# Kernel tuning notes

Hardware: AMD Instinct MI355X
Metric: run time of the kernel (lower is better)

The kernel has to match this reference:

```python
import jax, jax.numpy as jnp
import numpy as np

E = 8        # n_experts
K = 2        # top-k
DIM = 1024
HID = 2048   # swiglu hidden; fc1 out = 2*HID
B, T = 4, 2048


def setup_inputs() -> dict:
    key = jax.random.key(0)
    ks = jax.random.split(key, 7)
    s = 0.02
    return {
        "x": jax.random.normal(ks[0], (B, T, DIM), dtype=jnp.float32),
        "router_w": jax.random.normal(ks[1], (E, DIM), dtype=jnp.float32) * s,
        "router_b": jnp.zeros((E,), dtype=jnp.float32),
        "W1": jax.random.normal(ks[2], (E, DIM, 2 * HID), dtype=jnp.float32) * s,
        "b1": jnp.zeros((E, 2 * HID), dtype=jnp.float32),
        "W2": jax.random.normal(ks[3], (E, HID, DIM), dtype=jnp.float32) * s,
        "b2": jnp.zeros((E, DIM), dtype=jnp.float32),
    }


def _swiglu(h):
    h1, h2 = jnp.split(h, 2, axis=-1)
    return jax.nn.silu(h1) * h2


def reference(x, router_w, router_b, W1, b1, W2, b2):
    # Router: logits = Linear(dim, E), temperature = 1.0
    logits = jnp.einsum("btd,ed->bte", x, router_w) + router_b  # [B,T,E]
    topk_val, topk_idx = jax.lax.top_k(logits, K)               # [B,T,K]
    weights = jax.nn.softmax(topk_val, axis=-1)                 # softmax router
    # combine[b,t,e] = sum_k weights[b,t,k] * [topk_idx[b,t,k] == e]
    combine = jnp.sum(jax.nn.one_hot(topk_idx, E, dtype=x.dtype)
                      * weights[..., None], axis=-2)            # [B,T,E]
    out = jnp.zeros_like(x)
    # Fixed small loop over experts (structurally distinct weight slices).
    for e in range(E):
        h = jnp.einsum("btd,dh->bth", x, W1[e]) + b1[e]         # [B,T,2H]
        y = jnp.einsum("bth,hd->btd", _swiglu(h), W2[e]) + b2[e]
        out = out + combine[..., e:e + 1] * y
    return out
```

## Files before the change

### kernel.cpp

```cpp
#include <hip/hip_runtime.h>
#include <stdint.h>

typedef unsigned short u16;

#define E_    8
#define DIM_  1024
#define HID_  2048
#define H2_   4096
#define NTOK  8192
#define RTOK  32

typedef __attribute__((ext_vector_type(8))) short bf16x8;
typedef __attribute__((ext_vector_type(4))) float f32x4;

__device__ __forceinline__ u16 f2bf(float f) {
  uint32_t u = __builtin_bit_cast(uint32_t, f);
  uint32_t r = (u + 0x7FFFu + ((u >> 16) & 1u)) >> 16;
  return (u16)r;
}
__device__ __forceinline__ float bf2f(u16 u) {
  return __builtin_bit_cast(float, (uint32_t)u << 16);
}

__device__ __forceinline__ void gload16(const void* g, void* l) {
  __builtin_amdgcn_global_load_lds(
      (const __attribute__((address_space(1))) void*)g,
      (__attribute__((address_space(3))) void*)l, 16, 0, 0);
}


__global__ void cvt_x(const float* __restrict__ x, u16* __restrict__ xb, int n8) {
  int i = blockIdx.x * blockDim.x + threadIdx.x;
  if (i >= n8) return;
  const float4* p = (const float4*)(x + (size_t)i * 8);
  float4 a = p[0], b = p[1];
  union { u16 u[8]; uint4 v; } r;
  r.u[0] = f2bf(a.x); r.u[1] = f2bf(a.y); r.u[2] = f2bf(a.z); r.u[3] = f2bf(a.w);
  r.u[4] = f2bf(b.x); r.u[5] = f2bf(b.y); r.u[6] = f2bf(b.z); r.u[7] = f2bf(b.w);
  *(uint4*)(xb + (size_t)i * 8) = r.v;
}

__global__ void tconv(const float* __restrict__ src, u16* __restrict__ dst, int R, int C) {
  __shared__ float t[64][65];
  int e = blockIdx.z;
  int r0 = blockIdx.y * 64, c0 = blockIdx.x * 64;
  const float* s = src + (size_t)e * R * C;
  u16* d = dst + (size_t)e * R * C;
  int tid = threadIdx.x;
  int rr = tid >> 4, cc = (tid & 15) * 4;
#pragma unroll
  for (int p = 0; p < 4; ++p) {
    float4 v = *(const float4*)(s + (size_t)(r0 + p * 16 + rr) * C + c0 + cc);
    t[p * 16 + rr][cc + 0] = v.x; t[p * 16 + rr][cc + 1] = v.y;
    t[p * 16 + rr][cc + 2] = v.z; t[p * 16 + rr][cc + 3] = v.w;
  }
  __syncthreads();
  int cr = tid >> 3, rc = (tid & 7) * 8;
#pragma unroll
  for (int p = 0; p < 2; ++p) {
    union { u16 u[8]; uint4 v; } w;
#pragma unroll
    for (int j = 0; j < 8; ++j) w.u[j] = f2bf(t[rc + j][p * 32 + cr]);
    *(uint4*)(d + (size_t)(c0 + p * 32 + cr) * R + r0 + rc) = w.v;
  }
}


__global__ void router(const float* __restrict__ x, const float* __restrict__ rw,
                       const float* __restrict__ rb, int* __restrict__ counts,
                       int* __restrict__ btok, float* __restrict__ bw,
                       int* __restrict__ tokrec) {
  __shared__ float srw[E_ * DIM_];
  __shared__ float sb[E_];
  __shared__ int   hcnt[E_], hbase[E_];
  __shared__ int   te[RTOK * 2];
  __shared__ float twt[RTOK * 2];
  __shared__ int   tloc[RTOK * 2];

  int tid = threadIdx.x;
  for (int i = tid; i < E_ * DIM_ / 4; i += 256)
    ((float4*)srw)[i] = ((const float4*)rw)[i];
  if (tid < E_) { sb[tid] = rb[tid]; hcnt[tid] = 0; }
  __syncthreads();

  int wid = tid >> 6, lane = tid & 63;
#pragma unroll
  for (int s = 0; s < RTOK / 4; ++s) {
    int lt = wid * (RTOK / 4) + s;
    int t = blockIdx.x * RTOK + lt;
    const float* xt = x + (size_t)t * DIM_;
    float acc[8] = {0.f, 0.f, 0.f, 0.f, 0.f, 0.f, 0.f, 0.f};
#pragma unroll
    for (int it = 0; it < 4; ++it) {
      int d = it * 256 + lane * 4;
      float4 xv = *(const float4*)(xt + d);
#pragma unroll
      for (int e = 0; e < 8; ++e) {
        float4 rv = *(const float4*)(&srw[e * DIM_ + d]);
        acc[e] += xv.x * rv.x + xv.y * rv.y + xv.z * rv.z + xv.w * rv.w;
      }
    }
#pragma unroll
    for (int e = 0; e < 8; ++e)
#pragma unroll
      for (int off = 32; off; off >>= 1)
        acc[e] += __shfl_xor(acc[e], off, 64);
    if (lane == 0) {
      float v[8];
#pragma unroll
      for (int e = 0; e < 8; ++e) v[e] = acc[e] + sb[e];
      int i0 = 0;
#pragma unroll
      for (int e = 1; e < 8; ++e) if (v[e] > v[i0]) i0 = e;
      int i1 = (i0 == 0) ? 1 : 0;
#pragma unroll
      for (int e = 0; e < 8; ++e) if (e != i0 && v[e] > v[i1]) i1 = e;
      float w0 = 1.f / (1.f + expf(v[i1] - v[i0]));
      float w1 = 1.f - w0;
      int l0 = atomicAdd(&hcnt[i0], 1);
      int l1 = atomicAdd(&hcnt[i1], 1);
      te[lt * 2 + 0] = i0; twt[lt * 2 + 0] = w0; tloc[lt * 2 + 0] = l0;
      te[lt * 2 + 1] = i1; twt[lt * 2 + 1] = w1; tloc[lt * 2 + 1] = l1;
    }
  }
  __syncthreads();
  if (tid < E_) hbase[tid] = atomicAdd(&counts[tid], hcnt[tid]);
  __syncthreads();
  if (tid < RTOK * 2) {
    int e = te[tid];
    int p = hbase[e] + tloc[tid];
    int t = blockIdx.x * RTOK + (tid >> 1);
    btok[e * NTOK + p] = t;
    bw[e * NTOK + p] = twt[tid];
    tokrec[t * 2 + (tid & 1)] = (e << 13) | p;
  }
}


__launch_bounds__(256, 4)
__global__ void gemm1(const u16* __restrict__ xb, const u16* __restrict__ w1t,
                      const float* __restrict__ b1, const int* __restrict__ counts,
                      const int* __restrict__ btok, u16* __restrict__ hb) {
  int e = blockIdx.z, mblk = blockIdx.y, nblk = blockIdx.x;
  int cnt = counts[e];
  if (mblk * 128 >= cnt) return;
  int base = 0;
#pragma unroll
  for (int i = 0; i < 8; ++i) base += (i < e) ? counts[i] : 0;

  __shared__ u16 lA[128 * 64];
  __shared__ u16 lB[128 * 64];
  __shared__ int sTok[128];

  int tid = threadIdx.x, wid = tid >> 6, lane = tid & 63;
  if (tid < 128) {
    int gr = mblk * 128 + tid;
    sTok[tid] = (gr < cnt) ? btok[e * NTOK + gr] : btok[e * NTOK];
  }
  __syncthreads();

  f32x4 acc[4][4] = {};
  int wr = wid >> 1, wc = wid & 1;
  int l15 = lane & 15, lhi = lane >> 4;
  const size_t w1e = (size_t)e * H2_ * DIM_;

  int segsw = ((lane & 7) ^ ((lane >> 3) & 7)) * 8;
  const u16* gA[4];
  const u16* gB[4];
#pragma unroll
  for (int i = 0; i < 4; ++i) {
    int r = wid * 32 + i * 8 + (lane >> 3);
    gA[i] = xb + (size_t)sTok[r] * DIM_ + segsw;
    int gcol = nblk * 64 + (r >> 6) * 32 + (r & 31) + ((r >> 5) & 1) * 2048;
    gB[i] = w1t + w1e + (size_t)gcol * DIM_ + segsw;
  }
  int rxor = (l15 & 7) * 8;

  for (int kt = 0; kt < DIM_ / 64; ++kt) {
#pragma unroll
    for (int i = 0; i < 4; ++i)
      gload16(gA[i] + kt * 64, &lA[(wid * 32 + i * 8) * 64]);
#pragma unroll
    for (int i = 0; i < 4; ++i)
      gload16(gB[i] + kt * 64, &lB[(wid * 32 + i * 8) * 64]);
    __syncthreads();
#pragma unroll
    for (int ks = 0; ks < 2; ++ks) {
      int segrd = ((ks * 4 + lhi) * 8) ^ rxor;
      bf16x8 a[4], b[4];
#pragma unroll
      for (int m = 0; m < 4; ++m)
        a[m] = *(const bf16x8*)&lA[(wr * 64 + m * 16 + l15) * 64 + segrd];
#pragma unroll
      for (int n = 0; n < 4; ++n)
        b[n] = *(const bf16x8*)&lB[(wc * 64 + n * 16 + l15) * 64 + segrd];
#pragma unroll
      for (int m = 0; m < 4; ++m)
#pragma unroll
        for (int n = 0; n < 4; ++n)
          acc[m][n] = __builtin_amdgcn_mfma_f32_16x16x32_bf16(a[m], b[n], acc[m][n], 0, 0, 0);
    }
    __syncthreads();
  }

#pragma unroll
  for (int n = 0; n < 2; ++n) {
    int outcol = nblk * 64 + wc * 32 + n * 16 + l15;
    float bb1 = b1[e * H2_ + outcol];
    float bb2 = b1[e * H2_ + outcol + HID_];
#pragma unroll
    for (int m = 0; m < 4; ++m) {
#pragma unroll
      for (int j = 0; j < 4; ++j) {
        int rt = wr * 64 + m * 16 + lhi * 4 + j;
        int gr = mblk * 128 + rt;
        if (gr < cnt) {
          float h1 = acc[m][n][j] + bb1;
          float h2 = acc[m][n + 2][j] + bb2;
          float s = (h1 / (1.f + __expf(-h1))) * h2;
          hb[(size_t)(base + gr) * HID_ + outcol] = f2bf(s);
        }
      }
    }
  }
}


__launch_bounds__(256, 4)
__global__ void gemm2(const u16* __restrict__ hb, const u16* __restrict__ w2t,
                      const float* __restrict__ b2, const int* __restrict__ counts,
                      const float* __restrict__ bw, u16* __restrict__ ybuf) {
  int e = blockIdx.z, mblk = blockIdx.y, nblk = blockIdx.x;
  int cnt = counts[e];
  if (mblk * 128 >= cnt) return;
  int base = 0;
#pragma unroll
  for (int i = 0; i < 8; ++i) base += (i < e) ? counts[i] : 0;

  __shared__ u16 lA[128 * 64];
  __shared__ u16 lB[128 * 64];
  __shared__ float sW[128];

  int tid = threadIdx.x, wid = tid >> 6, lane = tid & 63;
  if (tid < 128) {
    int gr = mblk * 128 + tid;
    sW[tid] = (gr < cnt) ? bw[e * NTOK + gr] : 0.f;
  }
  __syncthreads();

  f32x4 acc[4][4] = {};
  int wr = wid >> 1, wc = wid & 1;
  int l15 = lane & 15, lhi = lane >> 4;

  int segsw = ((lane & 7) ^ ((lane >> 3) & 7)) * 8;
  const u16* gA[4];
  const u16* gB[4];
#pragma unroll
  for (int i = 0; i < 4; ++i) {
    int r = wid * 32 + i * 8 + (lane >> 3);
    gA[i] = hb + (size_t)(base + mblk * 128 + r) * HID_ + segsw;
    gB[i] = w2t + (size_t)e * DIM_ * HID_ + (size_t)(nblk * 128 + r) * HID_ + segsw;
  }
  int rxor = (l15 & 7) * 8;

  for (int kt = 0; kt < HID_ / 64; ++kt) {
#pragma unroll
    for (int i = 0; i < 4; ++i) {
      gload16(gA[i] + kt * 64, &lA[(wid * 32 + i * 8) * 64]);
      gload16(gB[i] + kt * 64, &lB[(wid * 32 + i * 8) * 64]);
    }
    __syncthreads();
#pragma unroll
    for (int ks = 0; ks < 2; ++ks) {
      int segrd = ((ks * 4 + lhi) * 8) ^ rxor;
      bf16x8 a[4], b[4];
#pragma unroll
      for (int m = 0; m < 4; ++m)
        a[m] = *(const bf16x8*)&lA[(wr * 64 + m * 16 + l15) * 64 + segrd];
#pragma unroll
      for (int n = 0; n < 4; ++n)
        b[n] = *(const bf16x8*)&lB[(wc * 64 + n * 16 + l15) * 64 + segrd];
#pragma unroll
      for (int m = 0; m < 4; ++m)
#pragma unroll
        for (int n = 0; n < 4; ++n)
          acc[m][n] = __builtin_amdgcn_mfma_f32_16x16x32_bf16(a[m], b[n], acc[m][n], 0, 0, 0);
    }
    __syncthreads();
  }

#pragma unroll
  for (int n = 0; n < 4; ++n) {
    int col = nblk * 128 + wc * 64 + n * 16 + l15;
    float bb = b2[e * DIM_ + col];
#pragma unroll
    for (int m = 0; m < 4; ++m) {
#pragma unroll
      for (int j = 0; j < 4; ++j) {
        int rt = wr * 64 + m * 16 + lhi * 4 + j;
        int gr = mblk * 128 + rt;
        if (gr < cnt)
          ybuf[(size_t)(base + gr) * DIM_ + col] = f2bf(sW[rt] * (acc[m][n][j] + bb));
      }
    }
  }
}


__global__ void combine(const u16* __restrict__ ybuf, const int* __restrict__ tokrec,
                        const int* __restrict__ counts, float* __restrict__ out) {
  __shared__ int sbase[8];
  int tid = threadIdx.x;
  if (tid == 0) {
    int b = 0;
#pragma unroll
    for (int e = 0; e < 8; ++e) { sbase[e] = b; b += counts[e]; }
  }
  __syncthreads();
  int t = blockIdx.x;
  int r0 = tokrec[t * 2 + 0], r1 = tokrec[t * 2 + 1];
  size_t s0 = (size_t)(sbase[r0 >> 13] + (r0 & 8191)) * DIM_;
  size_t s1 = (size_t)(sbase[r1 >> 13] + (r1 & 8191)) * DIM_;
  int c = tid * 4;
  ushort4 a = *(const ushort4*)(ybuf + s0 + c);
  ushort4 b = *(const ushort4*)(ybuf + s1 + c);
  float4 o;
  o.x = bf2f(a.x) + bf2f(b.x);
  o.y = bf2f(a.y) + bf2f(b.y);
  o.z = bf2f(a.z) + bf2f(b.z);
  o.w = bf2f(a.w) + bf2f(b.w);
  *(float4*)(out + (size_t)t * DIM_ + c) = o;
}


extern "C" void kernel_launch(void* const* d_in, const int* in_sizes, int n_in,
                              void* d_out, int out_size, void* d_ws, size_t ws_size,
                              hipStream_t stream) {
  const float* x  = (const float*)d_in[0];
  const float* rw = (const float*)d_in[1];
  const float* rb = (const float*)d_in[2];
  const float* W1 = (const float*)d_in[3];
  const float* b1 = (const float*)d_in[4];
  const float* W2 = (const float*)d_in[5];
  const float* b2 = (const float*)d_in[6];
  float* out = (float*)d_out;

  char* ws = (char*)d_ws;
  int*   counts = (int*)ws;
  int*   btok   = (int*)(ws + 256);
  float* bw     = (float*)(ws + 256 + 262144);
  int*   tokrec = (int*)(ws + 256 + 524288);
  u16* xb  = (u16*)(ws + (1u << 20));
  u16* w1t = xb  + (size_t)NTOK * DIM_;
  u16* w2t = w1t + (size_t)E_ * H2_ * DIM_;
  u16* hb  = w2t + (size_t)E_ * DIM_ * HID_;
  u16* ybuf = w1t;

  hipMemsetAsync(counts, 0, 8 * sizeof(int), stream);

  cvt_x<<<(NTOK * DIM_ / 8 + 255) / 256, 256, 0, stream>>>(x, xb, NTOK * DIM_ / 8);
  tconv<<<dim3(H2_ / 64, DIM_ / 64, E_), 256, 0, stream>>>(W1, w1t, DIM_, H2_);
  tconv<<<dim3(DIM_ / 64, HID_ / 64, E_), 256, 0, stream>>>(W2, w2t, HID_, DIM_);
  router<<<NTOK / RTOK, 256, 0, stream>>>(x, rw, rb, counts, btok, bw, tokrec);

  gemm1<<<dim3(H2_ / 128, NTOK / 128, E_), 256, 0, stream>>>(xb, w1t, b1, counts, btok, hb);
  gemm2<<<dim3(DIM_ / 128, NTOK / 128, E_), 256, 0, stream>>>(hb, w2t, b2, counts, bw, ybuf);
  combine<<<NTOK, 256, 0, stream>>>(ybuf, tokrec, counts, out);
}
```

Measured before the change: 401.7 us.

## Fuse x bf16 conversion into router and make expert slot assignment deterministic

Folds the fp32-to-bf16 conversion of x into the router so x is read once. The global atomic slot allocation is replaced by three kernels: per-block histograms, a single-block prefix scan, and a scatter pass. This removes the memset and the cvt_x launch and makes the token order within each expert deterministic. It adds two small launches, and the router now runs 1024 blocks that each reload the full router weight matrix into shared memory.

After: 381.1 us. -5.1%, faster.

```diff
diff --git a/kernel.cpp b/kernel.cpp
--- a/kernel.cpp
+++ b/kernel.cpp
@@ -8,7 +8,6 @@
 #define HID_  2048
 #define H2_   4096
 #define NTOK  8192
-#define RTOK  32
 
 typedef __attribute__((ext_vector_type(8))) short bf16x8;
 typedef __attribute__((ext_vector_type(4))) float f32x4;
@@ -28,17 +27,6 @@
       (__attribute__((address_space(3))) void*)l, 16, 0, 0);
 }
 
-
-__global__ void cvt_x(const float* __restrict__ x, u16* __restrict__ xb, int n8) {
-  int i = blockIdx.x * blockDim.x + threadIdx.x;
-  if (i >= n8) return;
-  const float4* p = (const float4*)(x + (size_t)i * 8);
-  float4 a = p[0], b = p[1];
-  union { u16 u[8]; uint4 v; } r;
-  r.u[0] = f2bf(a.x); r.u[1] = f2bf(a.y); r.u[2] = f2bf(a.z); r.u[3] = f2bf(a.w);
-  r.u[4] = f2bf(b.x); r.u[5] = f2bf(b.y); r.u[6] = f2bf(b.z); r.u[7] = f2bf(b.w);
-  *(uint4*)(xb + (size_t)i * 8) = r.v;
-}
 
 __global__ void tconv(const float* __restrict__ src, u16* __restrict__ dst, int R, int C) {
   __shared__ float t[64][65];
@@ -66,16 +54,13 @@
 }
 
 
-__global__ void router(const float* __restrict__ x, const float* __restrict__ rw,
-                       const float* __restrict__ rb, int* __restrict__ counts,
-                       int* __restrict__ btok, float* __restrict__ bw,
-                       int* __restrict__ tokrec) {
+__global__ void routerA(const float* __restrict__ x, const float* __restrict__ rw,
+                        const float* __restrict__ rb, u16* __restrict__ xb,
+                        int* __restrict__ gcnt, int2* __restrict__ te_l,
+                        float2* __restrict__ tw) {
   __shared__ float srw[E_ * DIM_];
   __shared__ float sb[E_];
-  __shared__ int   hcnt[E_], hbase[E_];
-  __shared__ int   te[RTOK * 2];
-  __shared__ float twt[RTOK * 2];
-  __shared__ int   tloc[RTOK * 2];
+  __shared__ int   hcnt[E_];
 
   int tid = threadIdx.x;
   for (int i = tid; i < E_ * DIM_ / 4; i += 256)
@@ -85,15 +70,17 @@
 
   int wid = tid >> 6, lane = tid & 63;
 #pragma unroll
-  for (int s = 0; s < RTOK / 4; ++s) {
-    int lt = wid * (RTOK / 4) + s;
-    int t = blockIdx.x * RTOK + lt;
+  for (int s = 0; s < 2; ++s) {
+    int t = blockIdx.x * 8 + wid * 2 + s;
     const float* xt = x + (size_t)t * DIM_;
     float acc[8] = {0.f, 0.f, 0.f, 0.f, 0.f, 0.f, 0.f, 0.f};
 #pragma unroll
     for (int it = 0; it < 4; ++it) {
       int d = it * 256 + lane * 4;
       float4 xv = *(const float4*)(xt + d);
+      ushort4 xo;
+      xo.x = f2bf(xv.x); xo.y = f2bf(xv.y); xo.z = f2bf(xv.z); xo.w = f2bf(xv.w);
+      *(ushort4*)(xb + (size_t)t * DIM_ + d) = xo;
 #pragma unroll
       for (int e = 0; e < 8; ++e) {
         float4 rv = *(const float4*)(&srw[e * DIM_ + d]);
@@ -116,24 +103,57 @@
 #pragma unroll
       for (int e = 0; e < 8; ++e) if (e != i0 && v[e] > v[i1]) i1 = e;
       float w0 = 1.f / (1.f + expf(v[i1] - v[i0]));
-      float w1 = 1.f - w0;
       int l0 = atomicAdd(&hcnt[i0], 1);
       int l1 = atomicAdd(&hcnt[i1], 1);
-      te[lt * 2 + 0] = i0; twt[lt * 2 + 0] = w0; tloc[lt * 2 + 0] = l0;
-      te[lt * 2 + 1] = i1; twt[lt * 2 + 1] = w1; tloc[lt * 2 + 1] = l1;
-    }
-  }
-  __syncthreads();
-  if (tid < E_) hbase[tid] = atomicAdd(&counts[tid], hcnt[tid]);
-  __syncthreads();
-  if (tid < RTOK * 2) {
-    int e = te[tid];
-    int p = hbase[e] + tloc[tid];
-    int t = blockIdx.x * RTOK + (tid >> 1);
-    btok[e * NTOK + p] = t;
-    bw[e * NTOK + p] = twt[tid];
-    tokrec[t * 2 + (tid & 1)] = (e << 13) | p;
-  }
+      te_l[t] = make_int2((i0 << 8) | l0, (i1 << 8) | l1);
+      tw[t] = make_float2(w0, 1.f - w0);
+    }
+  }
+  __syncthreads();
+  if (tid < E_) gcnt[tid * 1024 + blockIdx.x] = hcnt[tid];
+}
+
+
+__global__ void routerB(const int* __restrict__ gcnt, int* __restrict__ base_blk,
+                        int* __restrict__ counts) {
+  __shared__ int part[256];
+  int tid = threadIdx.x;
+#pragma unroll
+  for (int e = 0; e < 8; ++e) {
+    int4 v = *(const int4*)(gcnt + e * 1024 + tid * 4);
+    int s = v.x + v.y + v.z + v.w;
+    part[tid] = s;
+    __syncthreads();
+    for (int off = 1; off < 256; off <<= 1) {
+      int o = (tid >= off) ? part[tid - off] : 0;
+      __syncthreads();
+      part[tid] += o;
+      __syncthreads();
+    }
+    int ex = part[tid] - s;
+    int tot = part[255];
+    int4 b;
+    b.x = ex; b.y = ex + v.x; b.z = ex + v.x + v.y; b.w = ex + v.x + v.y + v.z;
+    *(int4*)(base_blk + e * 1024 + tid * 4) = b;
+    if (tid == 0) counts[e] = tot;
+    __syncthreads();
+  }
+}
+
+
+__global__ void routerC(const int2* __restrict__ te_l, const float2* __restrict__ tw,
+                        const int* __restrict__ base_blk, int* __restrict__ btok,
+                        float* __restrict__ bw, int* __restrict__ tokrec) {
+  int t = blockIdx.x * 256 + threadIdx.x;
+  int2 r = te_l[t];
+  float2 w = tw[t];
+  int b = t >> 3;
+  int e0 = r.x >> 8, l0 = r.x & 255;
+  int e1 = r.y >> 8, l1 = r.y & 255;
+  int p0 = base_blk[e0 * 1024 + b] + l0;
+  int p1 = base_blk[e1 * 1024 + b] + l1;
+  btok[e0 * NTOK + p0] = t; bw[e0 * NTOK + p0] = w.x; tokrec[t * 2 + 0] = (e0 << 13) | p0;
+  btok[e1 * NTOK + p1] = t; bw[e1 * NTOK + p1] = w.y; tokrec[t * 2 + 1] = (e1 << 13) | p1;
 }
 
 
@@ -346,22 +366,25 @@
   float* out = (float*)d_out;
 
   char* ws = (char*)d_ws;
-  int*   counts = (int*)ws;
-  int*   btok   = (int*)(ws + 256);
-  float* bw     = (float*)(ws + 256 + 262144);
-  int*   tokrec = (int*)(ws + 256 + 524288);
+  int*    counts   = (int*)ws;
+  int*    btok     = (int*)(ws + 256);
+  float*  bw       = (float*)(ws + 256 + 262144);
+  int*    tokrec   = (int*)(ws + 256 + 524288);
+  int*    gcnt     = (int*)(ws + 655360);
+  int*    base_blk = (int*)(ws + 688128);
+  int2*   te_l     = (int2*)(ws + 720896);
+  float2* tw       = (float2*)(ws + 786432);
   u16* xb  = (u16*)(ws + (1u << 20));
   u16* w1t = xb  + (size_t)NTOK * DIM_;
   u16* w2t = w1t + (size_t)E_ * H2_ * DIM_;
   u16* hb  = w2t + (size_t)E_ * DIM_ * HID_;
   u16* ybuf = w1t;
 
-  hipMemsetAsync(counts, 0, 8 * sizeof(int), stream);
-
-  cvt_x<<<(NTOK * DIM_ / 8 + 255) / 256, 256, 0, stream>>>(x, xb, NTOK * DIM_ / 8);
   tconv<<<dim3(H2_ / 64, DIM_ / 64, E_), 256, 0, stream>>>(W1, w1t, DIM_, H2_);
   tconv<<<dim3(DIM_ / 64, HID_ / 64, E_), 256, 0, stream>>>(W2, w2t, HID_, DIM_);
-  router<<<NTOK / RTOK, 256, 0, stream>>>(x, rw, rb, counts, btok, bw, tokrec);
+  routerA<<<1024, 256, 0, stream>>>(x, rw, rb, xb, gcnt, te_l, tw);
+  routerB<<<1, 256, 0, stream>>>(gcnt, base_blk, counts);
+  routerC<<<32, 256, 0, stream>>>(te_l, tw, base_blk, btok, bw, tokrec);
 
   gemm1<<<dim3(H2_ / 128, NTOK / 128, E_), 256, 0, stream>>>(xb, w1t, b1, counts, btok, hb);
   gemm2<<<dim3(DIM_ / 128, NTOK / 128, E_), 256, 0, stream>>>(hb, w2t, b2, counts, bw, ybuf);
```
